# Performance work log

Measured on AMD Instinct MI355X. Metric: run time of the kernel, lower is better.

The kernel has to match this reference:

```python
import jax, jax.numpy as jnp
import numpy as np
import math

B, D, L, Nh, Dk, Dv, K, CONV_NUM = 16, 256, 1024, 8, 32, 32, 7, 4
EPS = 1e-5


def _pos_encoding():
    # matches PosEncoder: freqs/phases per channel, sin(pos*freqs + phases), shape [D, L]
    idx = jnp.arange(D)
    i = idx.astype(jnp.float32)
    even = (idx % 2 == 0)
    freqs = jnp.where(even, 10000.0 ** (-i / D), -(10000.0 ** ((1.0 - i) / D)))
    phases = jnp.where(even, 0.0, math.pi / 2)
    pos = jnp.arange(L, dtype=jnp.float32)
    return jnp.sin(pos[None, :] * freqs[:, None] + phases[:, None])


def _layer_norm(x, g, b):
    # nn.LayerNorm([D, L]) on [B, D, L]: normalize over last two dims
    m = jnp.mean(x, axis=(1, 2), keepdims=True)
    v = jnp.mean((x - m) ** 2, axis=(1, 2), keepdims=True)
    return (x - m) * jax.lax.rsqrt(v + EPS) * g + b


def _ds_conv(x, dw, db, pw, pb):
    # depthwise conv1d (groups=D, same padding) + pointwise 1x1 conv
    y = jax.lax.conv_general_dilated(
        x, dw[:, None, :], window_strides=(1,), padding=[(K // 2, K // 2)],
        feature_group_count=D, dimension_numbers=('NCH', 'OIH', 'NCH'))
    y = y + db[None, :, None]
    return jnp.einsum('bdl,ed->bel', y, pw) + pb[None, :, None]


def setup_inputs() -> dict:
    key = jax.random.key(0)
    ks = jax.random.split(key, 12)

    def n(k, shape, scale):
        return jax.random.normal(k, shape, jnp.float32) * scale

    x = jax.random.normal(ks[0], (B, D, L), jnp.float32)
    mask = jax.random.randint(ks[1], (B, L), 0, 2).astype(jnp.int32)
    dw_w = n(ks[2], (CONV_NUM, D, K), 0.1)
    dw_b = jnp.zeros((CONV_NUM, D), jnp.float32)
    pw_w = n(ks[3], (CONV_NUM, D, D), 0.05)
    pw_b = jnp.zeros((CONV_NUM, D), jnp.float32)
    ln_g = jnp.ones((CONV_NUM + 2, D, L), jnp.float32)
    ln_b = jnp.zeros((CONV_NUM + 2, D, L), jnp.float32)
    Wq = n(ks[4], (Nh, D, Dk), 0.05)
    Wk = n(ks[5], (Nh, D, Dk), 0.05)
    Wv = n(ks[6], (Nh, D, Dv), 0.05)
    Wo = n(ks[7], (D, Dv * Nh), 0.05)
    fc_w = n(ks[8], (D, D), 0.05)
    fc_b = jnp.zeros((D,), jnp.float32)
    return dict(x=x, mask=mask, dw_w=dw_w, dw_b=dw_b, pw_w=pw_w, pw_b=pw_b,
                ln_g=ln_g, ln_b=ln_b, Wq=Wq, Wk=Wk, Wv=Wv, Wo=Wo,
                fc_w=fc_w, fc_b=fc_b)


def reference(x, mask, dw_w, dw_b, pw_w, pw_b, ln_g, ln_b, Wq, Wk, Wv, Wo, fc_w, fc_b):
    m = mask.astype(jnp.float32)  # [B, L]
    out = x + _pos_encoding()[None]
    res = out
    out = _layer_norm(out, ln_g[0], ln_b[0])
    for i in range(CONV_NUM):
        out = jax.nn.relu(_ds_conv(out, dw_w[i], dw_b[i], pw_w[i], pw_b[i])) + res
        # F.dropout in eval mode is identity
        res = out
        out = _layer_norm(out, ln_g[i + 1], ln_b[i + 1])
    # self attention (batched over heads instead of per-head loop; same math)
    xt = out.transpose(0, 2, 1)  # [B, L, D]
    q = jnp.einsum('bld,hdk->bhlk', xt, Wq)
    k = jnp.einsum('bld,hdk->bhlk', xt, Wk)
    v = jnp.einsum('bld,hdv->bhlv', xt, Wv)
    scores = jnp.einsum('bhqk,bhlk->bhql', q, k) * (1.0 / math.sqrt(Dk))
    hm = m[:, None, None, :]  # mask over key dim
    scores = scores * hm + (1.0 - hm) * (-1e30)
    attn = jax.nn.softmax(scores, axis=-1) * m[:, None, :, None]  # zero padded query rows
    heads = jnp.einsum('bhql,bhlv->bqhv', attn, v).reshape(B, L, Nh * Dv)  # head-major concat
    att_out = (heads @ Wo).transpose(0, 2, 1)  # [B, D, L]
    out = att_out + res
    res = out
    out = _layer_norm(out, ln_g[CONV_NUM + 1], ln_b[CONV_NUM + 1])
    out = jnp.einsum('bdl,ed->bel', out, fc_w) + fc_b[None, :, None]  # nn.Linear on [B,L,D]
    out = jax.nn.relu(out) + res
    return out
```

## Files before the change

### kernel.cpp

```cpp
#include <hip/hip_runtime.h>
#include <hip/hip_bf16.h>

#define NB 16
#define ND 256
#define NL 1024
#define NHH 8
#define NDK 32
#define NKW 7
#define NCONV 4
#define NPB (ND*NL)

constexpr float LN_EPS = 1e-5f;

typedef __attribute__((ext_vector_type(4))) float f32x4;
typedef __attribute__((ext_vector_type(4))) short bf16x4;
typedef __attribute__((ext_vector_type(8))) short bf16x8;

__device__ __forceinline__ short bf16s(float f){
  return (short)__builtin_bit_cast(unsigned short, __float2bfloat16(f));
}
__device__ __forceinline__ float b2f(short s){
  return __builtin_bit_cast(float, ((unsigned)(unsigned short)s) << 16);
}

__device__ __forceinline__ void ln_ab(const float* st, int slot, int b, float& mean, float& rstd){
  float s = 0.f, ss = 0.f;
  #pragma unroll
  for(int bin=0;bin<8;bin++){
    const float* p = st + ((size_t)((slot*NB+b)*8+bin))*32;
    s += p[0]; ss += p[1];
  }
  mean = s * (1.0f/NPB);
  float var = ss * (1.0f/NPB) - mean*mean;
  rstd = rsqrtf(var + LN_EPS);
}

__device__ __forceinline__ void stats_reduce(float s, float ss, float* stats, int slot, int b, int bin){
  __shared__ float red[8];
  #pragma unroll
  for(int o=32;o>0;o>>=1){ s += __shfl_down(s,o); ss += __shfl_down(ss,o); }
  int lane = threadIdx.x & 63, w = threadIdx.x >> 6;
  if(lane==0){ red[w*2]=s; red[w*2+1]=ss; }
  __syncthreads();
  if(threadIdx.x==0){
    float* p = stats + ((size_t)((slot*NB+b)*8+bin))*32;
    atomicAdd(&p[0], red[0]+red[2]+red[4]+red[6]);
    atomicAdd(&p[1], red[1]+red[3]+red[5]+red[7]);
  }
}

__global__ __launch_bounds__(256) void k_prep(const float* __restrict__ pw_w, const float* __restrict__ fc_w,
    const float* __restrict__ Wo, const float* __restrict__ Wq, const float* __restrict__ Wk,
    const float* __restrict__ Wv, const float* __restrict__ g, const float* __restrict__ btab,
    short* __restrict__ Wpwb, short* __restrict__ Wfcb, short* __restrict__ Wob, short* __restrict__ Wcat,
    short* __restrict__ gT, short* __restrict__ bT, float* __restrict__ postab){
  __shared__ float T[64][65];
  int blk = blockIdx.x, tid = threadIdx.x;
  if(blk < 256){
    int idx = blk*1024 + tid*4;
    f32x4 v = *(const f32x4*)(pw_w + idx);
    bf16x4 o;
    #pragma unroll
    for(int j=0;j<4;j++) o[j] = bf16s(v[j]);
    *(bf16x4*)(Wpwb + idx) = o;
  } else if(blk < 320){
    int idx = (blk-256)*1024 + tid*4;
    f32x4 v = *(const f32x4*)(fc_w + idx);
    bf16x4 o;
    #pragma unroll
    for(int j=0;j<4;j++) o[j] = bf16s(v[j]);
    *(bf16x4*)(Wfcb + idx) = o;
  } else if(blk < 384){
    int idx = (blk-320)*1024 + tid*4;
    int e = idx >> 8;
    bf16x4 o;
    #pragma unroll
    for(int j=0;j<4;j++){ int d = (idx+j)&255; o[j] = bf16s(Wo[d*ND + e]); }
    *(bf16x4*)(Wob + idx) = o;
  } else if(blk < 576){
    int idx = (blk-384)*1024 + tid*4;
    int og = idx >> 8, d = idx & 255;
    int seg = og >> 8, o = og & 255, h = o >> 5, k = o & 31;
    const float* W = (seg==0) ? Wq : ((seg==1) ? Wk : Wv);
    bf16x4 ov;
    #pragma unroll
    for(int j=0;j<4;j++) ov[j] = bf16s(W[((size_t)(h*ND + d + j))*NDK + k]);
    *(bf16x4*)(Wcat + idx) = ov;
  } else if(blk < 832){
    int d = blk - 576;
    int l = tid*4;
    const float LN1E4_OVER_D = 9.210340371976184f / (float)ND;
    float freq, phase;
    if((d & 1) == 0){ freq =  __expf(-(float)d*LN1E4_OVER_D);      phase = 0.f; }
    else            { freq = -__expf((1.f-(float)d)*LN1E4_OVER_D); phase = 1.5707963267948966f; }
    f32x4 o;
    #pragma unroll
    for(int j=0;j<4;j++) o[j] = sinf((float)(l+j)*freq + phase);
    *(f32x4*)(postab + ((size_t)d<<10) + l) = o;
  } else {
    int blk2 = blk - 832;
    int which = blk2 >> 6;
    int tile = blk2 & 63;
    int d0 = (tile & 3) << 6, l0 = (tile >> 2) << 6;
    const float* src = (which < 6) ? (g + (size_t)which*NPB) : (btab + (size_t)(which-6)*NPB);
    short* dst = (which < 6) ? (gT + (size_t)which*NPB) : (bT + (size_t)(which-6)*NPB);
    for(int i=tid;i<1024;i+=256){
      int dd = i>>4, l4 = i&15;
      f32x4 v = *(const f32x4*)(src + (size_t)(d0+dd)*NL + l0 + l4*4);
      #pragma unroll
      for(int j=0;j<4;j++) T[dd][l4*4+j] = v[j];
    }
    __syncthreads();
    for(int i=tid;i<1024;i+=256){
      int ll = i>>4, d4 = i&15;
      bf16x4 o;
      #pragma unroll
      for(int j=0;j<4;j++) o[j] = bf16s(T[d4*4+j][ll]);
      *(bf16x4*)(dst + (size_t)(l0+ll)*ND + d0 + d4*4) = o;
    }
  }
}

__global__ __launch_bounds__(256) void k_posadd(const float* __restrict__ x, const float* __restrict__ postab,
                                                short* __restrict__ Rb, float* __restrict__ stats){
  int blk = blockIdx.x;
  int lt = blk & 15, dt = (blk>>4)&3, b = blk>>6;
  int l0 = lt*64, d0 = dt*64;
  __shared__ float T[64][65];
  int tid = threadIdx.x;
  for(int i=tid;i<1024;i+=256){
    int dd = i>>4, l4 = i&15;
    int d = d0+dd;
    f32x4 xv = *(const f32x4*)(x + ((size_t)(b*ND+d)<<10) + l0 + l4*4);
    f32x4 pv = *(const f32x4*)(postab + ((size_t)d<<10) + l0 + l4*4);
    #pragma unroll
    for(int j=0;j<4;j++) T[dd][l4*4+j] = xv[j] + pv[j];
  }
  __syncthreads();
  float s=0.f, ss=0.f;
  for(int i=tid;i<1024;i+=256){
    int ll = i>>4, d4 = i&15;
    bf16x4 o;
    #pragma unroll
    for(int j=0;j<4;j++){
      short rs = bf16s(T[d4*4+j][ll]);
      o[j] = rs;
      float rv = b2f(rs);
      s += rv; ss += rv*rv;
    }
    *(bf16x4*)(Rb + ((size_t)(b*NL+l0+ll)<<8) + d0 + d4*4) = o;
  }
  stats_reduce(s, ss, stats, 0, b, blk & 7);
}

__global__ __launch_bounds__(256) void k_dwconvT(const short* __restrict__ Rb, const short* __restrict__ gT,
                                                 const short* __restrict__ bT, const float* __restrict__ w7,
                                                 const float* __restrict__ db, const float* __restrict__ stats,
                                                 short* __restrict__ Y, int slot){
  int blk = blockIdx.x;
  int lblk = blk & 63, b = blk >> 6;
  int tid = threadIdx.x;
  __shared__ float wLds[NKW][ND];
  __shared__ float dbLds[ND];
  for(int i=tid;i<ND*NKW;i+=256){ int d=i/NKW, q=i-d*NKW; wLds[q][d] = w7[i]; }
  dbLds[tid] = db[tid];
  float mean, rstd; ln_ab(stats, slot, b, mean, rstd);
  float mr = mean*rstd;
  __syncthreads();
  int d0 = (tid & 63)*4;
  int l0 = lblk*16 + (tid >> 6)*4;
  f32x4 ln[10];
  #pragma unroll
  for(int i=0;i<10;i++){
    int lp = l0 - 3 + i;
    if(lp >= 0 && lp < NL){
      bf16x4 v = *(const bf16x4*)(Rb + ((size_t)(b*NL+lp)<<8) + d0);
      bf16x4 gv = *(const bf16x4*)(gT + ((size_t)lp<<8) + d0);
      bf16x4 bv = *(const bf16x4*)(bT + ((size_t)lp<<8) + d0);
      f32x4 t;
      #pragma unroll
      for(int j=0;j<4;j++) t[j] = (b2f(v[j])*rstd - mr)*b2f(gv[j]) + b2f(bv[j]);
      ln[i] = t;
    } else ln[i] = (f32x4){0.f,0.f,0.f,0.f};
  }
  f32x4 dbv = *(const f32x4*)(&dbLds[d0]);
  #pragma unroll
  for(int jl=0;jl<4;jl++){
    f32x4 acc = dbv;
    #pragma unroll
    for(int q=0;q<NKW;q++){
      f32x4 wq = *(const f32x4*)(&wLds[q][d0]);
      #pragma unroll
      for(int j=0;j<4;j++) acc[j] += ln[jl+q][j]*wq[j];
    }
    bf16x4 o;
    #pragma unroll
    for(int j=0;j<4;j++) o[j] = bf16s(acc[j]);
    *(bf16x4*)(Y + ((size_t)(b*NL + l0 + jl)<<8) + d0) = o;
  }
}

__device__ __forceinline__ void stage_rows_bf16(short* dst, const short* src, int tid, int c){
  for(int i=tid;i<1024;i+=256){
    int rr = i>>4, kk = i&15;
    bf16x8 w = *(const bf16x8*)(src + (size_t)rr*ND + c*128 + kk*8);
    *(bf16x8*)((char*)dst + rr*256 + ((kk*16) ^ ((rr&7)<<4))) = w;
  }
}
__device__ __forceinline__ void stage_act_lnb(short* dst, const short* src, const short* g, const short* bt,
                                              float mean, float rstd, int tid, int c){
  float mr = mean*rstd;
  for(int i=tid;i<1024;i+=256){
    int ll = i>>4, kk = i&15;
    size_t off = (size_t)ll*ND + c*128 + kk*8;
    bf16x8 v = *(const bf16x8*)(src + off);
    bf16x8 gv = *(const bf16x8*)(g + off);
    bf16x8 bv = *(const bf16x8*)(bt + off);
    bf16x8 o;
    #pragma unroll
    for(int j=0;j<8;j++) o[j] = bf16s((b2f(v[j])*rstd - mr)*b2f(gv[j]) + b2f(bv[j]));
    *(bf16x8*)((char*)dst + ll*256 + ((kk*16) ^ ((ll&7)<<4))) = o;
  }
}
__device__ __forceinline__ void mfma_core(const short* As, const short* Bs, int wm, int wn,
                                          int lq, int gg, f32x4 acc[2][2]){
  #pragma unroll
  for(int t=0;t<4;t++){
    bf16x8 a[2], bb[2];
    #pragma unroll
    for(int m=0;m<2;m++){
      int row = wm*32 + m*16 + lq;
      a[m] = *(const bf16x8*)((const char*)As + row*256 + ((t*64 + gg*16) ^ ((row&7)<<4)));
    }
    #pragma unroll
    for(int n=0;n<2;n++){
      int row = wn*32 + n*16 + lq;
      bb[n] = *(const bf16x8*)((const char*)Bs + row*256 + ((t*64 + gg*16) ^ ((row&7)<<4)));
    }
    #pragma unroll
    for(int m=0;m<2;m++)
      #pragma unroll
      for(int n=0;n<2;n++)
        acc[m][n] = __builtin_amdgcn_mfma_f32_16x16x32_bf16(a[m], bb[n], acc[m][n], 0,0,0);
  }
}

#define GEMM_PROLOGUE() \
  int blk = blockIdx.x; \
  int lt = blk & 15, et = (blk>>4)&3, b = blk>>6; \
  int l0 = lt*64, e0 = et*64; \
  int tid = threadIdx.x; \
  int w = tid>>6, lane = tid&63, lq = lane&15, gg = lane>>4; \
  int wm = w&1, wn = w>>1; \
  __shared__ short As[8192], Bs[8192]; \
  f32x4 acc[2][2]; \
  acc[0][0]=acc[0][1]=acc[1][0]=acc[1][1] = (f32x4){0.f,0.f,0.f,0.f};

__global__ __launch_bounds__(256) void k_pw(const short* __restrict__ Y, const short* __restrict__ Wb,
                                            const float* __restrict__ bias, short* __restrict__ Rb,
                                            float* __restrict__ stats, int slot_out){
  GEMM_PROLOGUE();
  const short* Asrc = Y + ((size_t)(b*NL)+l0)*ND;
  const short* Bsrc = Wb + (size_t)e0*ND;
  for(int c=0;c<2;c++){
    __syncthreads();
    stage_rows_bf16(As, Asrc, tid, c);
    stage_rows_bf16(Bs, Bsrc, tid, c);
    __syncthreads();
    mfma_core(As, Bs, wm, wn, lq, gg, acc);
  }
  float s=0.f, ss=0.f;
  #pragma unroll
  for(int n=0;n<2;n++){
    int e = e0 + wn*32 + n*16 + lq;
    float bv = bias[e];
    #pragma unroll
    for(int m=0;m<2;m++){
      #pragma unroll
      for(int r=0;r<4;r++){
        int l = l0 + wm*32 + m*16 + gg*4 + r;
        size_t ix = (size_t)(b*NL+l)*ND + e;
        float v = fmaxf(acc[m][n][r] + bv, 0.f);
        float rr = b2f(Rb[ix]) + v;
        short rs = bf16s(rr);
        Rb[ix] = rs;
        float r2 = b2f(rs);
        s += r2; ss += r2*r2;
      }
    }
  }
  stats_reduce(s, ss, stats, slot_out, b, blk & 7);
}

__global__ __launch_bounds__(256) void k_qkvf(const short* __restrict__ Rb, const short* __restrict__ gT,
                                              const short* __restrict__ bT, const float* __restrict__ stats,
                                              const short* __restrict__ Wcat, short* __restrict__ Qb,
                                              short* __restrict__ Kb, short* __restrict__ Vb){
  int blk = blockIdx.x;
  int lt = blk & 15;
  int tmp = blk >> 4;
  int et = tmp % 12, b = tmp / 12;
  int l0 = lt*64, e0g = et*64;
  int seg = et >> 2;
  int tid = threadIdx.x;
  int w = tid>>6, lane = tid&63, lq = lane&15, gg = lane>>4;
  int wm = w&1, wn = w>>1;
  __shared__ short As[8192], Bs[8192];
  f32x4 acc[2][2];
  acc[0][0]=acc[0][1]=acc[1][0]=acc[1][1] = (f32x4){0.f,0.f,0.f,0.f};
  float mean, rstd; ln_ab(stats, 4, b, mean, rstd);
  const short* Asrc = Rb + ((size_t)(b*NL)+l0)*ND;
  const short* gs = gT + (size_t)l0*ND;
  const short* bs = bT + (size_t)l0*ND;
  const short* Bsrc = Wcat + (size_t)e0g*ND;
  for(int c=0;c<2;c++){
    __syncthreads();
    stage_act_lnb(As, Asrc, gs, bs, mean, rstd, tid, c);
    stage_rows_bf16(Bs, Bsrc, tid, c);
    __syncthreads();
    mfma_core(As, Bs, wm, wn, lq, gg, acc);
  }
  #pragma unroll
  for(int n=0;n<2;n++){
    int eo = (et&3)*64 + wn*32 + n*16 + lq;
    int h = eo>>5, dk = eo&31;
    if(seg < 2){
      short* outp = (seg==0) ? Qb : Kb;
      #pragma unroll
      for(int m=0;m<2;m++){
        #pragma unroll
        for(int r=0;r<4;r++){
          int l = l0 + wm*32 + m*16 + gg*4 + r;
          outp[((size_t)(b*NHH+h)*NL + l)*NDK + dk] = bf16s(acc[m][n][r]);
        }
      }
    } else {
      #pragma unroll
      for(int m=0;m<2;m++){
        int lb = l0 + wm*32 + m*16 + gg*4;
        bf16x4 pk;
        #pragma unroll
        for(int r=0;r<4;r++) pk[r] = bf16s(acc[m][n][r]);
        *(bf16x4*)(Vb + ((size_t)(b*NHH+h)*NDK + dk)*NL + lb) = pk;
      }
    }
  }
}

__global__ __launch_bounds__(256) void k_attn(const short* __restrict__ Qb, const short* __restrict__ Kb,
                                              const short* __restrict__ Vt, const int* __restrict__ mask,
                                              short* __restrict__ heads){
  int blk = blockIdx.x;
  int qblk = blk >> 7, bh = blk & 127;
  int b = bh >> 3, h = bh & 7;
  int tid = threadIdx.x;
  int w = tid >> 6, lane = tid & 63;
  int lq = lane & 15, gg = lane >> 4;

  __shared__ short Ks[64][40];
  __shared__ short Vs[32][72];
  __shared__ short Ps[4][16][40];
  __shared__ float msh[64];

  int qrow = qblk*64 + w*16 + lq;
  bf16x8 qf = *(const bf16x8*)(Qb + ((size_t)bh*NL + qrow)*NDK + gg*8);

  bf16x8 ones;
  #pragma unroll
  for(int j=0;j<8;j++) ones[j] = (short)0x3F80;

  f32x4 zero = {0.f,0.f,0.f,0.f};
  f32x4 o0 = zero, o1 = zero, o2 = zero;
  const float scale = 0.17677669529663687f;

  for(int t0=0; t0<NL; t0+=64){
    __syncthreads();
    {
      int key = tid >> 2, c = tid & 3;
      *(bf16x8*)(&Ks[key][c*8]) = *(const bf16x8*)(Kb + ((size_t)bh*NL + t0 + key)*NDK + c*8);
      int v = tid >> 3, ch = tid & 7;
      *(bf16x8*)(&Vs[v][ch*8]) = *(const bf16x8*)(Vt + ((size_t)bh*NDK + v)*NL + t0 + ch*8);
      if(tid < 64) msh[tid] = ((float)mask[b*NL + t0 + tid] - 1.f) * 1e30f;
    }
    __syncthreads();
    #pragma unroll
    for(int sub=0; sub<2; sub++){
      bf16x8 a0 = *(const bf16x8*)(&Ks[sub*32 + lq][gg*8]);
      bf16x8 a1 = *(const bf16x8*)(&Ks[sub*32 + 16 + lq][gg*8]);
      f32x4 c0 = __builtin_amdgcn_mfma_f32_16x16x32_bf16(a0, qf, zero, 0, 0, 0);
      f32x4 c1 = __builtin_amdgcn_mfma_f32_16x16x32_bf16(a1, qf, zero, 0, 0, 0);
      bf16x4 p0, p1;
      #pragma unroll
      for(int r=0;r<4;r++){
        float pv0 = __expf(__builtin_fmaf(c0[r], scale, msh[sub*32 + gg*4 + r]));
        p0[r] = bf16s(pv0);
        float pv1 = __expf(__builtin_fmaf(c1[r], scale, msh[sub*32 + 16 + gg*4 + r]));
        p1[r] = bf16s(pv1);
      }
      *(bf16x4*)(&Ps[w][lq][gg*4])      = p0;
      *(bf16x4*)(&Ps[w][lq][16 + gg*4]) = p1;
      bf16x8 pf = *(const bf16x8*)(&Ps[w][lq][gg*8]);
      bf16x8 b0 = *(const bf16x8*)(&Vs[lq][sub*32 + gg*8]);
      bf16x8 b1 = *(const bf16x8*)(&Vs[16 + lq][sub*32 + gg*8]);
      o0 = __builtin_amdgcn_mfma_f32_16x16x32_bf16(pf, b0, o0, 0, 0, 0);
      o1 = __builtin_amdgcn_mfma_f32_16x16x32_bf16(pf, b1, o1, 0, 0, 0);
      o2 = __builtin_amdgcn_mfma_f32_16x16x32_bf16(pf, ones, o2, 0, 0, 0);
    }
  }
  #pragma unroll
  for(int r=0;r<4;r++){
    int ql = gg*4 + r;
    int qg = qblk*64 + w*16 + ql;
    float mq = (float)mask[b*NL + qg];
    float sc = mq / o2[r];
    short* op = heads + ((size_t)(b*NL + qg))*(NHH*NDK) + h*NDK;
    op[lq]      = bf16s(o0[r]*sc);
    op[16 + lq] = bf16s(o1[r]*sc);
  }
}

__global__ __launch_bounds__(256) void k_wo(const short* __restrict__ H, const short* __restrict__ Wb,
                                            short* __restrict__ Rb, float* __restrict__ stats){
  GEMM_PROLOGUE();
  const short* Asrc = H + ((size_t)(b*NL)+l0)*ND;
  const short* Bsrc = Wb + (size_t)e0*ND;
  for(int c=0;c<2;c++){
    __syncthreads();
    stage_rows_bf16(As, Asrc, tid, c);
    stage_rows_bf16(Bs, Bsrc, tid, c);
    __syncthreads();
    mfma_core(As, Bs, wm, wn, lq, gg, acc);
  }
  float s=0.f, ss=0.f;
  #pragma unroll
  for(int n=0;n<2;n++){
    int e = e0 + wn*32 + n*16 + lq;
    #pragma unroll
    for(int m=0;m<2;m++){
      #pragma unroll
      for(int r=0;r<4;r++){
        int l = l0 + wm*32 + m*16 + gg*4 + r;
        size_t ix = (size_t)(b*NL+l)*ND + e;
        float rr = b2f(Rb[ix]) + acc[m][n][r];
        short rs = bf16s(rr);
        Rb[ix] = rs;
        float r2 = b2f(rs);
        s += r2; ss += r2*r2;
      }
    }
  }
  stats_reduce(s, ss, stats, 5, b, blk & 7);
}

__global__ __launch_bounds__(256) void k_fc(const short* __restrict__ Rb, const short* __restrict__ gT,
                                            const short* __restrict__ bT, const float* __restrict__ stats,
                                            const short* __restrict__ Wb, const float* __restrict__ bias,
                                            float* __restrict__ out){
  GEMM_PROLOGUE();
  float mean, rstd; ln_ab(stats, 5, b, mean, rstd);
  const short* Asrc = Rb + ((size_t)(b*NL)+l0)*ND;
  const short* gs = gT + (size_t)l0*ND;
  const short* bs = bT + (size_t)l0*ND;
  const short* Bsrc = Wb + (size_t)e0*ND;
  for(int c=0;c<2;c++){
    __syncthreads();
    stage_act_lnb(As, Asrc, gs, bs, mean, rstd, tid, c);
    stage_rows_bf16(Bs, Bsrc, tid, c);
    __syncthreads();
    mfma_core(As, Bs, wm, wn, lq, gg, acc);
  }
  #pragma unroll
  for(int n=0;n<2;n++){
    int e = e0 + wn*32 + n*16 + lq;
    float bv = bias[e];
    #pragma unroll
    for(int m=0;m<2;m++){
      int lb = l0 + wm*32 + m*16 + gg*4;
      f32x4 ov;
      #pragma unroll
      for(int r=0;r<4;r++){
        float v = fmaxf(acc[m][n][r] + bv, 0.f);
        ov[r] = v + b2f(Rb[(size_t)(b*NL+lb+r)*ND + e]);
      }
      *(f32x4*)(out + (size_t)(b*ND+e)*NL + lb) = ov;
    }
  }
}

extern "C" void kernel_launch(void* const* d_in, const int* in_sizes, int n_in,
                              void* d_out, int out_size, void* d_ws, size_t ws_size,
                              hipStream_t stream){
  const float* x    = (const float*)d_in[0];
  const int*   mask = (const int*)d_in[1];
  const float* dw_w = (const float*)d_in[2];
  const float* dw_b = (const float*)d_in[3];
  const float* pw_w = (const float*)d_in[4];
  const float* pw_b = (const float*)d_in[5];
  const float* ln_g = (const float*)d_in[6];
  const float* ln_b = (const float*)d_in[7];
  const float* Wq   = (const float*)d_in[8];
  const float* Wk   = (const float*)d_in[9];
  const float* Wv   = (const float*)d_in[10];
  const float* Wo   = (const float*)d_in[11];
  const float* fc_w = (const float*)d_in[12];
  const float* fc_b = (const float*)d_in[13];

  float* ws     = (float*)d_ws;
  float* stats  = ws;
  float* postab = ws + 98304;
  short* Rb     = (short*)(ws + 360448);
  short* Yb     = (short*)(ws + 2457600);
  short* Qb     = (short*)(ws + 4554752);
  short* Kb     = (short*)(ws + 6651904);
  short* Vb     = (short*)(ws + 8749056);
  short* gT     = (short*)(ws + 10846208);
  short* bT     = (short*)(ws + 11632640);
  short* Wpwb   = (short*)(ws + 12419072);
  short* Wfcb   = (short*)(ws + 12550144);
  short* Wob    = (short*)(ws + 12582912);
  short* Wcat   = (short*)(ws + 12615680);

  hipMemsetAsync(stats, 0, 98304*sizeof(float), stream);
  k_prep<<<1600,256,0,stream>>>(pw_w, fc_w, Wo, Wq, Wk, Wv, ln_g, ln_b,
                                Wpwb, Wfcb, Wob, Wcat, gT, bT, postab);
  k_posadd<<<1024,256,0,stream>>>(x, postab, Rb, stats);
  for(int i=0;i<NCONV;i++){
    k_dwconvT<<<1024,256,0,stream>>>(Rb, gT + (size_t)i*NPB, bT + (size_t)i*NPB,
                                     dw_w + i*ND*NKW, dw_b + i*ND, stats, Yb, i);
    k_pw<<<1024,256,0,stream>>>(Yb, Wpwb + (size_t)i*65536, pw_b + i*ND, Rb, stats, i+1);
  }
  k_qkvf<<<3072,256,0,stream>>>(Rb, gT + (size_t)4*NPB, bT + (size_t)4*NPB, stats, Wcat, Qb, Kb, Vb);
  k_attn<<<2048,256,0,stream>>>(Qb, Kb, Vb, mask, Yb);
  k_wo<<<1024,256,0,stream>>>(Yb, Wob, Rb, stats);
  k_fc<<<1024,256,0,stream>>>(Rb, gT + (size_t)5*NPB, bT + (size_t)5*NPB, stats, Wfcb, fc_b, (float*)d_out);
}
```

Baseline: 304.7 us.

## Fuse depthwise conv with pointwise GEMM; read attention K/V directly from global

Removes the separate depthwise-conv kernel. The LayerNorm plus 7-tap depthwise conv is computed inside the pointwise GEMM's A-tile staging, and results ping-pong between two residual buffers. This drops one launch and one full Y round-trip through HBM per conv layer. The cost is that each of the four output-column blocks recomputes the conv over the same 64-row tile, and halo rows are reloaded. Separately, the attention kernel stops staging K/V and the mask through shared memory with block syncs and loads fragments straight from global/L2 instead.

New measurement: 382.0 us. 25.4% more time.

```diff
diff --git a/kernel.cpp b/kernel.cpp
--- a/kernel.cpp
+++ b/kernel.cpp
@@ -52,8 +52,9 @@
 __global__ __launch_bounds__(256) void k_prep(const float* __restrict__ pw_w, const float* __restrict__ fc_w,
     const float* __restrict__ Wo, const float* __restrict__ Wq, const float* __restrict__ Wk,
     const float* __restrict__ Wv, const float* __restrict__ g, const float* __restrict__ btab,
+    const float* __restrict__ dw_w,
     short* __restrict__ Wpwb, short* __restrict__ Wfcb, short* __restrict__ Wob, short* __restrict__ Wcat,
-    short* __restrict__ gT, short* __restrict__ bT, float* __restrict__ postab){
+    short* __restrict__ gT, short* __restrict__ bT, float* __restrict__ postab, float* __restrict__ wTt){
   __shared__ float T[64][65];
   int blk = blockIdx.x, tid = threadIdx.x;
   if(blk < 256){
@@ -97,7 +98,7 @@
     #pragma unroll
     for(int j=0;j<4;j++) o[j] = sinf((float)(l+j)*freq + phase);
     *(f32x4*)(postab + ((size_t)d<<10) + l) = o;
-  } else {
+  } else if(blk < 1600){
     int blk2 = blk - 832;
     int which = blk2 >> 6;
     int tile = blk2 & 63;
@@ -117,6 +118,17 @@
       #pragma unroll
       for(int j=0;j<4;j++) o[j] = bf16s(T[d4*4+j][ll]);
       *(bf16x4*)(dst + (size_t)(l0+ll)*ND + d0 + d4*4) = o;
+    }
+  } else {
+    int base = (blk-1600)*1024 + tid*4;
+    #pragma unroll
+    for(int j=0;j<4;j++){
+      int idx = base + j;
+      if(idx < NCONV*NKW*ND){
+        int layer = idx / (NKW*ND), rem = idx % (NKW*ND);
+        int q = rem >> 8, d = rem & 255;
+        wTt[idx] = dw_w[(layer*ND + d)*NKW + q];
+      }
     }
   }
 }
@@ -153,53 +165,6 @@
   stats_reduce(s, ss, stats, 0, b, blk & 7);
 }
 
-__global__ __launch_bounds__(256) void k_dwconvT(const short* __restrict__ Rb, const short* __restrict__ gT,
-                                                 const short* __restrict__ bT, const float* __restrict__ w7,
-                                                 const float* __restrict__ db, const float* __restrict__ stats,
-                                                 short* __restrict__ Y, int slot){
-  int blk = blockIdx.x;
-  int lblk = blk & 63, b = blk >> 6;
-  int tid = threadIdx.x;
-  __shared__ float wLds[NKW][ND];
-  __shared__ float dbLds[ND];
-  for(int i=tid;i<ND*NKW;i+=256){ int d=i/NKW, q=i-d*NKW; wLds[q][d] = w7[i]; }
-  dbLds[tid] = db[tid];
-  float mean, rstd; ln_ab(stats, slot, b, mean, rstd);
-  float mr = mean*rstd;
-  __syncthreads();
-  int d0 = (tid & 63)*4;
-  int l0 = lblk*16 + (tid >> 6)*4;
-  f32x4 ln[10];
-  #pragma unroll
-  for(int i=0;i<10;i++){
-    int lp = l0 - 3 + i;
-    if(lp >= 0 && lp < NL){
-      bf16x4 v = *(const bf16x4*)(Rb + ((size_t)(b*NL+lp)<<8) + d0);
-      bf16x4 gv = *(const bf16x4*)(gT + ((size_t)lp<<8) + d0);
-      bf16x4 bv = *(const bf16x4*)(bT + ((size_t)lp<<8) + d0);
-      f32x4 t;
-      #pragma unroll
-      for(int j=0;j<4;j++) t[j] = (b2f(v[j])*rstd - mr)*b2f(gv[j]) + b2f(bv[j]);
-      ln[i] = t;
-    } else ln[i] = (f32x4){0.f,0.f,0.f,0.f};
-  }
-  f32x4 dbv = *(const f32x4*)(&dbLds[d0]);
-  #pragma unroll
-  for(int jl=0;jl<4;jl++){
-    f32x4 acc = dbv;
-    #pragma unroll
-    for(int q=0;q<NKW;q++){
-      f32x4 wq = *(const f32x4*)(&wLds[q][d0]);
-      #pragma unroll
-      for(int j=0;j<4;j++) acc[j] += ln[jl+q][j]*wq[j];
-    }
-    bf16x4 o;
-    #pragma unroll
-    for(int j=0;j<4;j++) o[j] = bf16s(acc[j]);
-    *(bf16x4*)(Y + ((size_t)(b*NL + l0 + jl)<<8) + d0) = o;
-  }
-}
-
 __device__ __forceinline__ void stage_rows_bf16(short* dst, const short* src, int tid, int c){
   for(int i=tid;i<1024;i+=256){
     int rr = i>>4, kk = i&15;
@@ -245,26 +210,66 @@
   }
 }
 
-#define GEMM_PROLOGUE() \
-  int blk = blockIdx.x; \
-  int lt = blk & 15, et = (blk>>4)&3, b = blk>>6; \
-  int l0 = lt*64, e0 = et*64; \
-  int tid = threadIdx.x; \
-  int w = tid>>6, lane = tid&63, lq = lane&15, gg = lane>>4; \
-  int wm = w&1, wn = w>>1; \
-  __shared__ short As[8192], Bs[8192]; \
-  f32x4 acc[2][2]; \
+__device__ __forceinline__ f32x4 lnrow4(const short* __restrict__ Rin, const short* __restrict__ gT,
+                                        const short* __restrict__ bT, int b, int lp, int dof,
+                                        float rstd, float mr){
+  f32x4 t = {0.f,0.f,0.f,0.f};
+  if((unsigned)lp < NL){
+    bf16x4 v  = *(const bf16x4*)(Rin + ((size_t)(b*NL+lp)<<8) + dof);
+    bf16x4 gv = *(const bf16x4*)(gT + ((size_t)lp<<8) + dof);
+    bf16x4 bv = *(const bf16x4*)(bT + ((size_t)lp<<8) + dof);
+    #pragma unroll
+    for(int j=0;j<4;j++) t[j] = (b2f(v[j])*rstd - mr)*b2f(gv[j]) + b2f(bv[j]);
+  }
+  return t;
+}
+
+__global__ __launch_bounds__(256) void k_cpw(const short* __restrict__ Rin, const short* __restrict__ gT,
+    const short* __restrict__ bT, const float* __restrict__ wT, const float* __restrict__ db,
+    const short* __restrict__ Wb, const float* __restrict__ bias, short* __restrict__ Rout,
+    float* __restrict__ stats, int slot_in, int slot_out){
+  int blk = blockIdx.x;
+  int lt = blk & 15, et = (blk>>4)&3, b = blk>>6;
+  int l0 = lt*64, e0 = et*64;
+  int tid = threadIdx.x;
+  int w = tid>>6, lane = tid&63, lq = lane&15, gg = lane>>4;
+  int wm = w&1, wn = w>>1;
+  __shared__ short As[8192], Bs[8192];
+  f32x4 acc[2][2];
   acc[0][0]=acc[0][1]=acc[1][0]=acc[1][1] = (f32x4){0.f,0.f,0.f,0.f};
-
-__global__ __launch_bounds__(256) void k_pw(const short* __restrict__ Y, const short* __restrict__ Wb,
-                                            const float* __restrict__ bias, short* __restrict__ Rb,
-                                            float* __restrict__ stats, int slot_out){
-  GEMM_PROLOGUE();
-  const short* Asrc = Y + ((size_t)(b*NL)+l0)*ND;
+  float mean, rstd; ln_ab(stats, slot_in, b, mean, rstd);
+  float mr = mean*rstd;
+  int kk4 = tid & 31, lg8 = tid >> 5;
   const short* Bsrc = Wb + (size_t)e0*ND;
   for(int c=0;c<2;c++){
     __syncthreads();
-    stage_rows_bf16(As, Asrc, tid, c);
+    {
+      int dof = c*128 + kk4*4;
+      f32x4 wv[7];
+      #pragma unroll
+      for(int q=0;q<7;q++) wv[q] = *(const f32x4*)(wT + q*ND + dof);
+      f32x4 dbv = *(const f32x4*)(db + dof);
+      int lbase = l0 + lg8*8;
+      f32x4 ring[7];
+      #pragma unroll
+      for(int j=0;j<7;j++) ring[j] = lnrow4(Rin, gT, bT, b, lbase-3+j, dof, rstd, mr);
+      #pragma unroll
+      for(int ol=0;ol<8;ol++){
+        f32x4 y = dbv;
+        #pragma unroll
+        for(int q=0;q<7;q++){
+          f32x4 rg = ring[(ol+q)%7];
+          #pragma unroll
+          for(int j=0;j<4;j++) y[j] += rg[j]*wv[q][j];
+        }
+        int row = lg8*8 + ol;
+        bf16x4 o;
+        #pragma unroll
+        for(int j=0;j<4;j++) o[j] = bf16s(y[j]);
+        *(bf16x4*)((char*)As + row*256 + ((kk4*8) ^ ((row&7)<<4))) = o;
+        if(ol<7) ring[ol%7] = lnrow4(Rin, gT, bT, b, lbase+4+ol, dof, rstd, mr);
+      }
+    }
     stage_rows_bf16(Bs, Bsrc, tid, c);
     __syncthreads();
     mfma_core(As, Bs, wm, wn, lq, gg, acc);
@@ -281,9 +286,9 @@
         int l = l0 + wm*32 + m*16 + gg*4 + r;
         size_t ix = (size_t)(b*NL+l)*ND + e;
         float v = fmaxf(acc[m][n][r] + bv, 0.f);
-        float rr = b2f(Rb[ix]) + v;
+        float rr = b2f(Rin[ix]) + v;
         short rs = bf16s(rr);
-        Rb[ix] = rs;
+        Rout[ix] = rs;
         float r2 = b2f(rs);
         s += r2; ss += r2*r2;
       }
@@ -357,10 +362,7 @@
   int w = tid >> 6, lane = tid & 63;
   int lq = lane & 15, gg = lane >> 4;
 
-  __shared__ short Ks[64][40];
-  __shared__ short Vs[32][72];
   __shared__ short Ps[4][16][40];
-  __shared__ float msh[64];
 
   int qrow = qblk*64 + w*16 + lq;
   bf16x8 qf = *(const bf16x8*)(Qb + ((size_t)bh*NL + qrow)*NDK + gg*8);
@@ -373,35 +375,36 @@
   f32x4 o0 = zero, o1 = zero, o2 = zero;
   const float scale = 0.17677669529663687f;
 
+  const short* Kbase = Kb + (size_t)bh*NL*NDK;
+  const short* V0 = Vt + ((size_t)bh*NDK + lq)*NL;
+  const short* V1 = Vt + ((size_t)bh*NDK + 16 + lq)*NL;
+  const int* mb = mask + b*NL;
+
   for(int t0=0; t0<NL; t0+=64){
-    __syncthreads();
-    {
-      int key = tid >> 2, c = tid & 3;
-      *(bf16x8*)(&Ks[key][c*8]) = *(const bf16x8*)(Kb + ((size_t)bh*NL + t0 + key)*NDK + c*8);
-      int v = tid >> 3, ch = tid & 7;
-      *(bf16x8*)(&Vs[v][ch*8]) = *(const bf16x8*)(Vt + ((size_t)bh*NDK + v)*NL + t0 + ch*8);
-      if(tid < 64) msh[tid] = ((float)mask[b*NL + t0 + tid] - 1.f) * 1e30f;
-    }
-    __syncthreads();
     #pragma unroll
     for(int sub=0; sub<2; sub++){
-      bf16x8 a0 = *(const bf16x8*)(&Ks[sub*32 + lq][gg*8]);
-      bf16x8 a1 = *(const bf16x8*)(&Ks[sub*32 + 16 + lq][gg*8]);
+      int kb = t0 + sub*32;
+      bf16x8 a0 = *(const bf16x8*)(Kbase + (size_t)(kb + lq)*NDK + gg*8);
+      bf16x8 a1 = *(const bf16x8*)(Kbase + (size_t)(kb + 16 + lq)*NDK + gg*8);
+      int4 mi0 = *(const int4*)(mb + kb + gg*4);
+      int4 mi1 = *(const int4*)(mb + kb + 16 + gg*4);
+      int ma0[4] = {mi0.x, mi0.y, mi0.z, mi0.w};
+      int ma1[4] = {mi1.x, mi1.y, mi1.z, mi1.w};
       f32x4 c0 = __builtin_amdgcn_mfma_f32_16x16x32_bf16(a0, qf, zero, 0, 0, 0);
       f32x4 c1 = __builtin_amdgcn_mfma_f32_16x16x32_bf16(a1, qf, zero, 0, 0, 0);
       bf16x4 p0, p1;
       #pragma unroll
       for(int r=0;r<4;r++){
-        float pv0 = __expf(__builtin_fmaf(c0[r], scale, msh[sub*32 + gg*4 + r]));
+        float pv0 = __expf(__builtin_fmaf(c0[r], scale, ((float)ma0[r]-1.f)*1e30f));
         p0[r] = bf16s(pv0);
-        float pv1 = __expf(__builtin_fmaf(c1[r], scale, msh[sub*32 + 16 + gg*4 + r]));
+        float pv1 = __expf(__builtin_fmaf(c1[r], scale, ((float)ma1[r]-1.f)*1e30f));
         p1[r] = bf16s(pv1);
       }
       *(bf16x4*)(&Ps[w][lq][gg*4])      = p0;
       *(bf16x4*)(&Ps[w][lq][16 + gg*4]) = p1;
       bf16x8 pf = *(const bf16x8*)(&Ps[w][lq][gg*8]);
-      bf16x8 b0 = *(const bf16x8*)(&Vs[lq][sub*32 + gg*8]);
-      bf16x8 b1 = *(const bf16x8*)(&Vs[16 + lq][sub*32 + gg*8]);
+      bf16x8 b0 = *(const bf16x8*)(V0 + kb + gg*8);
+      bf16x8 b1 = *(const bf16x8*)(V1 + kb + gg*8);
       o0 = __builtin_amdgcn_mfma_f32_16x16x32_bf16(pf, b0, o0, 0, 0, 0);
       o1 = __builtin_amdgcn_mfma_f32_16x16x32_bf16(pf, b1, o1, 0, 0, 0);
       o2 = __builtin_amdgcn_mfma_f32_16x16x32_bf16(pf, ones, o2, 0, 0, 0);
@@ -421,7 +424,15 @@
 
 __global__ __launch_bounds__(256) void k_wo(const short* __restrict__ H, const short* __restrict__ Wb,
                                             short* __restrict__ Rb, float* __restrict__ stats){
-  GEMM_PROLOGUE();
+  int blk = blockIdx.x;
+  int lt = blk & 15, et = (blk>>4)&3, b = blk>>6;
+  int l0 = lt*64, e0 = et*64;
+  int tid = threadIdx.x;
+  int w = tid>>6, lane = tid&63, lq = lane&15, gg = lane>>4;
+  int wm = w&1, wn = w>>1;
+  __shared__ short As[8192], Bs[8192];
+  f32x4 acc[2][2];
+  acc[0][0]=acc[0][1]=acc[1][0]=acc[1][1] = (f32x4){0.f,0.f,0.f,0.f};
   const short* Asrc = H + ((size_t)(b*NL)+l0)*ND;
   const short* Bsrc = Wb + (size_t)e0*ND;
   for(int c=0;c<2;c++){
@@ -456,7 +467,15 @@
                                             const short* __restrict__ bT, const float* __restrict__ stats,
                                             const short* __restrict__ Wb, const float* __restrict__ bias,
                                             float* __restrict__ out){
-  GEMM_PROLOGUE();
+  int blk = blockIdx.x;
+  int lt = blk & 15, et = (blk>>4)&3, b = blk>>6;
+  int l0 = lt*64, e0 = et*64;
+  int tid = threadIdx.x;
+  int w = tid>>6, lane = tid&63, lq = lane&15, gg = lane>>4;
+  int wm = w&1, wn = w>>1;
+  __shared__ short As[8192], Bs[8192];
+  f32x4 acc[2][2];
+  acc[0][0]=acc[0][1]=acc[1][0]=acc[1][1] = (f32x4){0.f,0.f,0.f,0.f};
   float mean, rstd; ln_ab(stats, 5, b, mean, rstd);
   const short* Asrc = Rb + ((size_t)(b*NL)+l0)*ND;
   const short* gs = gT + (size_t)l0*ND;
@@ -508,29 +527,35 @@
   float* ws     = (float*)d_ws;
   float* stats  = ws;
   float* postab = ws + 98304;
-  short* Rb     = (short*)(ws + 360448);
-  short* Yb     = (short*)(ws + 2457600);
-  short* Qb     = (short*)(ws + 4554752);
-  short* Kb     = (short*)(ws + 6651904);
-  short* Vb     = (short*)(ws + 8749056);
-  short* gT     = (short*)(ws + 10846208);
-  short* bT     = (short*)(ws + 11632640);
-  short* Wpwb   = (short*)(ws + 12419072);
-  short* Wfcb   = (short*)(ws + 12550144);
-  short* Wob    = (short*)(ws + 12582912);
-  short* Wcat   = (short*)(ws + 12615680);
+  short* Rb0    = (short*)(ws + 360448);
+  short* Rb1    = (short*)(ws + 2457600);
+  short* Hb     = (short*)(ws + 4554752);
+  short* Qb     = (short*)(ws + 6651904);
+  short* Kb     = (short*)(ws + 8749056);
+  short* Vb     = (short*)(ws + 10846208);
+  short* gT     = (short*)(ws + 12943360);
+  short* bT     = (short*)(ws + 13729792);
+  short* Wpwb   = (short*)(ws + 14516224);
+  short* Wfcb   = (short*)(ws + 14647296);
+  short* Wob    = (short*)(ws + 14680064);
+  short* Wcat   = (short*)(ws + 14712832);
+  float* wTt    = ws + 14811136;
 
   hipMemsetAsync(stats, 0, 98304*sizeof(float), stream);
-  k_prep<<<1600,256,0,stream>>>(pw_w, fc_w, Wo, Wq, Wk, Wv, ln_g, ln_b,
-                                Wpwb, Wfcb, Wob, Wcat, gT, bT, postab);
-  k_posadd<<<1024,256,0,stream>>>(x, postab, Rb, stats);
+  k_prep<<<1608,256,0,stream>>>(pw_w, fc_w, Wo, Wq, Wk, Wv, ln_g, ln_b, dw_w,
+                                Wpwb, Wfcb, Wob, Wcat, gT, bT, postab, wTt);
+  k_posadd<<<1024,256,0,stream>>>(x, postab, Rb0, stats);
+  short* Pin = Rb0;
+  short* Pout = Rb1;
   for(int i=0;i<NCONV;i++){
-    k_dwconvT<<<1024,256,0,stream>>>(Rb, gT + (size_t)i*NPB, bT + (size_t)i*NPB,
-                                     dw_w + i*ND*NKW, dw_b + i*ND, stats, Yb, i);
-    k_pw<<<1024,256,0,stream>>>(Yb, Wpwb + (size_t)i*65536, pw_b + i*ND, Rb, stats, i+1);
-  }
-  k_qkvf<<<3072,256,0,stream>>>(Rb, gT + (size_t)4*NPB, bT + (size_t)4*NPB, stats, Wcat, Qb, Kb, Vb);
-  k_attn<<<2048,256,0,stream>>>(Qb, Kb, Vb, mask, Yb);
-  k_wo<<<1024,256,0,stream>>>(Yb, Wob, Rb, stats);
-  k_fc<<<1024,256,0,stream>>>(Rb, gT + (size_t)5*NPB, bT + (size_t)5*NPB, stats, Wfcb, fc_b, (float*)d_out);
-}
+    k_cpw<<<1024,256,0,stream>>>(Pin, gT + (size_t)i*NPB, bT + (size_t)i*NPB,
+                                 wTt + (size_t)i*NKW*ND, dw_b + i*ND,
+                                 Wpwb + (size_t)i*65536, pw_b + i*ND,
+                                 Pout, stats, i, i+1);
+    short* t = Pin; Pin = Pout; Pout = t;
+  }
+  k_qkvf<<<3072,256,0,stream>>>(Pin, gT + (size_t)4*NPB, bT + (size_t)4*NPB, stats, Wcat, Qb, Kb, Vb);
+  k_attn<<<2048,256,0,stream>>>(Qb, Kb, Vb, mask, Hb);
+  k_wo<<<1024,256,0,stream>>>(Hb, Wob, Pin, stats);
+  k_fc<<<1024,256,0,stream>>>(Pin, gT + (size_t)5*NPB, bT + (size_t)5*NPB, stats, Wfcb, fc_b, (float*)d_out);
+}
```
